# Performance work log

Measured on AMD Instinct MI355X. Metric: run time of the kernel, lower is better.

Reference implementation:

```python
import jax, jax.numpy as jnp
import numpy as np

B, C, W, H = 4, 256, 64, 64
CQ = C // 8


def setup_inputs() -> dict:
    key = jax.random.key(0)
    ks = jax.random.split(key, 8)
    s = 1.0 / np.sqrt(C)
    return {
        "x": jax.random.normal(ks[0], (B, C, W, H), dtype=jnp.float32),
        "Wq": jax.random.normal(ks[1], (CQ, C), dtype=jnp.float32) * s,
        "bq": jnp.zeros((CQ,), dtype=jnp.float32),
        "Wk": jax.random.normal(ks[2], (CQ, C), dtype=jnp.float32) * s,
        "bk": jnp.zeros((CQ,), dtype=jnp.float32),
        "Wv": jax.random.normal(ks[3], (C, C), dtype=jnp.float32) * s,
        "bv": jnp.zeros((C,), dtype=jnp.float32),
        "gamma": jnp.zeros((1,), dtype=jnp.float32),
    }


def reference(x, Wq, bq, Wk, bk, Wv, bv, gamma):
    b, c, w, h = x.shape
    n = w * h
    xf = x.reshape(b, c, n)  # [B, C, N] flattened spatial
    # 1x1 convs are channel-wise linear maps
    q = jnp.einsum("dc,bcn->bnd", Wq, xf) + bq  # [B, N, C//8]
    k = jnp.einsum("dc,bcn->bdn", Wk, xf) + bk[None, :, None]  # [B, C//8, N]
    v = jnp.einsum("dc,bcn->bdn", Wv, xf) + bv[None, :, None]  # [B, C, N]
    attn = jax.nn.softmax(jnp.einsum("bnd,bdm->bnm", q, k), axis=-1)  # [B, N, N]
    # out[b, c, n] = sum_m v[b, c, m] * attn[b, n, m]
    out = jnp.einsum("bdm,bnm->bdn", v, attn).reshape(b, c, w, h)
    return gamma[0] * out + x
```

## Files before the change

### kernel.cpp

```cpp
#include <hip/hip_runtime.h>
#include <hip/hip_bf16.h>

#define CC 256
#define NN 4096
#define CQ 32
#define LOG2E 1.4426950408889634f

using short8 = __attribute__((ext_vector_type(8))) short;
using f32x4  = __attribute__((ext_vector_type(4))) float;

static __device__ __forceinline__ short f2bf(float f) {
  __hip_bfloat16 h = __float2bfloat16(f);
  return *reinterpret_cast<short*>(&h);
}

__global__ __launch_bounds__(256) void prep_kernel(
    const float* __restrict__ Wq, const float* __restrict__ Wk,
    const float* __restrict__ Wv, __hip_bfloat16* __restrict__ Wf)
{
  int t = blockIdx.x*256 + threadIdx.x;
  int lane = t & 63, frag = t >> 6;
  int tile = frag >> 3, kc = frag & 7;
  int l15 = lane & 15, quad = lane >> 4;
  int R = tile*16 + l15;
  int k0 = kc*32 + quad*8;
  const float* src;
  if (R < 32)       src = Wq + (size_t)R*CC + k0;
  else if (R < 64)  src = Wk + (size_t)(R-32)*CC + k0;
  else              src = Wv + (size_t)(R-64)*CC + k0;
  float4 a = *(const float4*)(src);
  float4 c = *(const float4*)(src + 4);
  short8 o;
  o[0]=f2bf(a.x); o[1]=f2bf(a.y); o[2]=f2bf(a.z); o[3]=f2bf(a.w);
  o[4]=f2bf(c.x); o[5]=f2bf(c.y); o[6]=f2bf(c.z); o[7]=f2bf(c.w);
  *reinterpret_cast<short8*>(reinterpret_cast<short*>(Wf) + (size_t)t*8) = o;
}

__global__ __launch_bounds__(512, 2) void qkv_kernel(
    const float* __restrict__ x, const __hip_bfloat16* __restrict__ Wf,
    const float* __restrict__ bq, const float* __restrict__ bk,
    const float* __restrict__ bv,
    __hip_bfloat16* __restrict__ qb, __hip_bfloat16* __restrict__ kb,
    __hip_bfloat16* __restrict__ vb)
{
  const int b  = blockIdx.y;
  const int n0 = blockIdx.x * 64;
  const int tid = threadIdx.x;
  const int lane = tid & 63;
  const int w = __builtin_amdgcn_readfirstlane(tid >> 6);
  const int l15 = lane & 15, quad = lane >> 4;

  __shared__ __align__(16) short Xs[64][264];
  __shared__ __align__(16) short Vr[8][16][72];

  const int sn = tid & 63, cg8 = tid >> 6;
  const float* xcol = x + (size_t)b*CC*NN + n0 + sn;
#pragma unroll
  for (int it = 0; it < 4; it++) {
    int cbase = it*64 + cg8*8;
    float v[8];
#pragma unroll
    for (int j = 0; j < 8; j++) v[j] = xcol[(size_t)(cbase + j)*NN];
    short8 sv;
#pragma unroll
    for (int j = 0; j < 8; j++) sv[j] = f2bf(v[j]);
    *reinterpret_cast<short8*>(&Xs[sn][cbase]) = sv;
  }
  __syncthreads();

  const short* wfp = reinterpret_cast<const short*>(Wf);

#define QKV_TILE(T) { \
    const int t_ = (T); \
    short8 Af[8]; \
    _Pragma("unroll") \
    for (int kc = 0; kc < 8; kc++) \
      Af[kc] = *(const short8*)(wfp + ((size_t)(t_*8 + kc)*64 + lane)*8); \
    f32x4 ac0 = {0.f,0.f,0.f,0.f}, ac1 = {0.f,0.f,0.f,0.f}; \
    f32x4 ac2 = {0.f,0.f,0.f,0.f}, ac3 = {0.f,0.f,0.f,0.f}; \
    _Pragma("unroll") \
    for (int kc = 0; kc < 8; kc++) { \
      short8 B0 = *(const short8*)(&Xs[     l15][kc*32 + quad*8]); \
      short8 B1 = *(const short8*)(&Xs[16 + l15][kc*32 + quad*8]); \
      short8 B2 = *(const short8*)(&Xs[32 + l15][kc*32 + quad*8]); \
      short8 B3 = *(const short8*)(&Xs[48 + l15][kc*32 + quad*8]); \
      ac0 = __builtin_amdgcn_mfma_f32_16x16x32_bf16(Af[kc], B0, ac0, 0,0,0); \
      ac1 = __builtin_amdgcn_mfma_f32_16x16x32_bf16(Af[kc], B1, ac1, 0,0,0); \
      ac2 = __builtin_amdgcn_mfma_f32_16x16x32_bf16(Af[kc], B2, ac2, 0,0,0); \
      ac3 = __builtin_amdgcn_mfma_f32_16x16x32_bf16(Af[kc], B3, ac3, 0,0,0); \
    } \
    if (t_ < 2) { \
      int d0 = t_*16; \
      _Pragma("unroll") \
      for (int r = 0; r < 4; r++) { \
        int d = d0 + quad*4 + r; float bb = bq[d]; \
        qb[(size_t)b*NN*CQ + (size_t)(n0      + l15)*CQ + d] = __float2bfloat16(LOG2E*(ac0[r] + bb)); \
        qb[(size_t)b*NN*CQ + (size_t)(n0 + 16 + l15)*CQ + d] = __float2bfloat16(LOG2E*(ac1[r] + bb)); \
        qb[(size_t)b*NN*CQ + (size_t)(n0 + 32 + l15)*CQ + d] = __float2bfloat16(LOG2E*(ac2[r] + bb)); \
        qb[(size_t)b*NN*CQ + (size_t)(n0 + 48 + l15)*CQ + d] = __float2bfloat16(LOG2E*(ac3[r] + bb)); \
      } \
    } else if (t_ < 4) { \
      int d0 = (t_-2)*16; \
      _Pragma("unroll") \
      for (int r = 0; r < 4; r++) { \
        int d = d0 + quad*4 + r; float bb = bk[d]; \
        kb[(size_t)b*NN*CQ + (size_t)(n0      + l15)*CQ + d] = __float2bfloat16(ac0[r] + bb); \
        kb[(size_t)b*NN*CQ + (size_t)(n0 + 16 + l15)*CQ + d] = __float2bfloat16(ac1[r] + bb); \
        kb[(size_t)b*NN*CQ + (size_t)(n0 + 32 + l15)*CQ + d] = __float2bfloat16(ac2[r] + bb); \
        kb[(size_t)b*NN*CQ + (size_t)(n0 + 48 + l15)*CQ + d] = __float2bfloat16(ac3[r] + bb); \
      } \
    } else { \
      int rv0 = (t_-4)*16; \
      _Pragma("unroll") \
      for (int r = 0; r < 4; r++) { \
        float bb = bv[rv0 + quad*4 + r]; \
        Vr[w][quad*4 + r][     l15] = f2bf(ac0[r] + bb); \
        Vr[w][quad*4 + r][16 + l15] = f2bf(ac1[r] + bb); \
        Vr[w][quad*4 + r][32 + l15] = f2bf(ac2[r] + bb); \
        Vr[w][quad*4 + r][48 + l15] = f2bf(ac3[r] + bb); \
      } \
      int row = lane >> 2, cb = (lane & 3)*16; \
      short8 t0 = *(const short8*)(&Vr[w][row][cb]); \
      short8 t1 = *(const short8*)(&Vr[w][row][cb + 8]); \
      *(short8*)(vb + ((size_t)b*CC + rv0 + row)*NN + n0 + cb)     = t0; \
      *(short8*)(vb + ((size_t)b*CC + rv0 + row)*NN + n0 + cb + 8) = t1; \
    } }

  QKV_TILE(2*w);
  QKV_TILE(2*w + 1);
  if (w < 4) { QKV_TILE(16 + w); }
#undef QKV_TILE
}

__global__ __launch_bounds__(512, 2) void attn_kernel(
    const __hip_bfloat16* __restrict__ qb, const __hip_bfloat16* __restrict__ kb,
    const __hip_bfloat16* __restrict__ vb,
    const float* __restrict__ x, const float* __restrict__ gamma,
    float* __restrict__ out)
{
  const int Bk = blockIdx.x;
  const int b = (Bk & 7) >> 1;
  const int n0 = ((Bk >> 3)*2 + (Bk & 1)) * 64;
  const int tid = threadIdx.x;
  const int lane = tid & 63;
  const int w = __builtin_amdgcn_readfirstlane(tid >> 6);
  const int sg = w & 3;
  const int mh = w >> 2;
  const int l15 = lane & 15, quad = lane >> 4;

  __shared__ __align__(16) short Vs[256][72];
  __shared__ __align__(16) short Ps[64][72];
  __shared__ float Lbuf2[2][64];

  const short* qbase = (const short*)qb + (size_t)b*NN*CQ;
  const short* kbase = (const short*)kb + (size_t)b*NN*CQ;
  const short* vbase = (const short*)vb + (size_t)b*CC*NN;

  short8 aq = *(const short8*)(qbase + (size_t)(n0 + sg*16 + l15)*CQ + quad*8);

  const int vr = tid >> 1, sh = tid & 1;

  short8 vf0, vf1, vf2, vf3, kf0, kf1;
#pragma unroll
  for (int j = 0; j < 4; j++) {
    short8 t = *(const short8*)(vbase + (size_t)vr*NN + sh*32 + j*8);
    if (j == 0) vf0 = t; else if (j == 1) vf1 = t; else if (j == 2) vf2 = t; else vf3 = t;
  }
  kf0 = *(const short8*)(kbase + (size_t)(mh*32 +      l15)*CQ + quad*8);
  kf1 = *(const short8*)(kbase + (size_t)(mh*32 + 16 + l15)*CQ + quad*8);
  *(short8*)(&Vs[vr][sh*32 +  0]) = vf0;
  *(short8*)(&Vs[vr][sh*32 +  8]) = vf1;
  *(short8*)(&Vs[vr][sh*32 + 16]) = vf2;
  *(short8*)(&Vs[vr][sh*32 + 24]) = vf3;

  f32x4 acc[4][4];
#pragma unroll
  for (int cg = 0; cg < 4; cg++)
#pragma unroll
    for (int ng = 0; ng < 4; ng++) acc[cg][ng] = (f32x4){0.f,0.f,0.f,0.f};
  float lsum[4] = {0.f,0.f,0.f,0.f};

  __syncthreads();

  for (int T = 0; T < 64; T++) {
    short8 nv0, nv1, nv2, nv3, nk0, nk1;
    if (T < 63) {
      const short* vp = vbase + (size_t)vr*NN + (T+1)*64 + sh*32;
      nv0 = *(const short8*)(vp);
      nv1 = *(const short8*)(vp + 8);
      nv2 = *(const short8*)(vp + 16);
      nv3 = *(const short8*)(vp + 24);
      nk0 = *(const short8*)(kbase + (size_t)((T+1)*64 + mh*32 +      l15)*CQ + quad*8);
      nk1 = *(const short8*)(kbase + (size_t)((T+1)*64 + mh*32 + 16 + l15)*CQ + quad*8);
    }

    f32x4 z = {0.f,0.f,0.f,0.f};
    f32x4 S0 = __builtin_amdgcn_mfma_f32_16x16x32_bf16(aq, kf0, z, 0,0,0);
    f32x4 S1 = __builtin_amdgcn_mfma_f32_16x16x32_bf16(aq, kf1, z, 0,0,0);
#pragma unroll
    for (int r = 0; r < 4; r++) {
      float e0 = __builtin_amdgcn_exp2f(S0[r]);
      float e1 = __builtin_amdgcn_exp2f(S1[r]);
      lsum[r] += e0 + e1;
      Ps[sg*16 + quad*4 + r][mh*32 +      l15] = f2bf(e0);
      Ps[sg*16 + quad*4 + r][mh*32 + 16 + l15] = f2bf(e1);
    }
    __syncthreads();

    short8 ap0 = *(const short8*)(&Ps[     l15][mh*32 + quad*8]);
    short8 ap1 = *(const short8*)(&Ps[16 + l15][mh*32 + quad*8]);
    short8 ap2 = *(const short8*)(&Ps[32 + l15][mh*32 + quad*8]);
    short8 ap3 = *(const short8*)(&Ps[48 + l15][mh*32 + quad*8]);
#pragma unroll
    for (int cg = 0; cg < 4; cg++) {
      short8 av = *(const short8*)(&Vs[sg*64 + cg*16 + l15][mh*32 + quad*8]);
      acc[cg][0] = __builtin_amdgcn_mfma_f32_16x16x32_bf16(av, ap0, acc[cg][0], 0,0,0);
      acc[cg][1] = __builtin_amdgcn_mfma_f32_16x16x32_bf16(av, ap1, acc[cg][1], 0,0,0);
      acc[cg][2] = __builtin_amdgcn_mfma_f32_16x16x32_bf16(av, ap2, acc[cg][2], 0,0,0);
      acc[cg][3] = __builtin_amdgcn_mfma_f32_16x16x32_bf16(av, ap3, acc[cg][3], 0,0,0);
    }
    __syncthreads();

    if (T < 63) {
      *(short8*)(&Vs[vr][sh*32 +  0]) = nv0;
      *(short8*)(&Vs[vr][sh*32 +  8]) = nv1;
      *(short8*)(&Vs[vr][sh*32 + 16]) = nv2;
      *(short8*)(&Vs[vr][sh*32 + 24]) = nv3;
      kf0 = nk0; kf1 = nk1;
    }
  }

#pragma unroll
  for (int r = 0; r < 4; r++) {
    float s = lsum[r];
    s += __shfl_xor(s, 1); s += __shfl_xor(s, 2);
    s += __shfl_xor(s, 4); s += __shfl_xor(s, 8);
    if (l15 == 0) Lbuf2[mh][sg*16 + quad*4 + r] = s;
  }

  float* poolf = reinterpret_cast<float*>(&Vs[0][0]);
  __syncthreads();
#pragma unroll
  for (int g = 0; g < 2; g++) {
    if (mh == 1 && (sg >> 1) == g) {
#pragma unroll
      for (int cg = 0; cg < 4; cg++)
#pragma unroll
        for (int ng = 0; ng < 4; ng++)
#pragma unroll
          for (int r = 0; r < 4; r++)
            poolf[(sg & 1)*4096 + (cg*16 + quad*4 + r)*64 + ng*16 + l15] = acc[cg][ng][r];
    }
    __syncthreads();
    if (mh == 0 && (sg >> 1) == g) {
#pragma unroll
      for (int cg = 0; cg < 4; cg++)
#pragma unroll
        for (int ng = 0; ng < 4; ng++)
#pragma unroll
          for (int r = 0; r < 4; r++)
            acc[cg][ng][r] += poolf[(sg & 1)*4096 + (cg*16 + quad*4 + r)*64 + ng*16 + l15];
    }
    __syncthreads();
  }

  if (mh == 0) {
    const float gm = gamma[0];
    float Lv[4];
#pragma unroll
    for (int ng = 0; ng < 4; ng++)
      Lv[ng] = 1.0f / (Lbuf2[0][ng*16 + l15] + Lbuf2[1][ng*16 + l15]);
#pragma unroll
    for (int cg = 0; cg < 4; cg++) {
#pragma unroll
      for (int ng = 0; ng < 4; ng++) {
#pragma unroll
        for (int r = 0; r < 4; r++) {
          size_t idx = ((size_t)b*CC + sg*64 + cg*16 + quad*4 + r)*NN + n0 + ng*16 + l15;
          out[idx] = gm * acc[cg][ng][r] * Lv[ng] + x[idx];
        }
      }
    }
  }
}

extern "C" void kernel_launch(void* const* d_in, const int* in_sizes, int n_in,
                              void* d_out, int out_size, void* d_ws, size_t ws_size,
                              hipStream_t stream) {
  const float* x     = (const float*)d_in[0];
  const float* Wq    = (const float*)d_in[1];
  const float* bq    = (const float*)d_in[2];
  const float* Wk    = (const float*)d_in[3];
  const float* bk    = (const float*)d_in[4];
  const float* Wv    = (const float*)d_in[5];
  const float* bv    = (const float*)d_in[6];
  const float* gamma = (const float*)d_in[7];
  float* out = (float*)d_out;

  char* ws = (char*)d_ws;
  if (ws_size < (11u << 20)) return;
  __hip_bfloat16* qb = (__hip_bfloat16*)(ws);
  __hip_bfloat16* kb = (__hip_bfloat16*)(ws + (1u << 20));
  __hip_bfloat16* vb = (__hip_bfloat16*)(ws + (2u << 20));
  __hip_bfloat16* Wf = (__hip_bfloat16*)(ws + (10u << 20));

  prep_kernel<<<dim3(40), 256, 0, stream>>>(Wq, Wk, Wv, Wf);
  qkv_kernel<<<dim3(64, 4), 512, 0, stream>>>(x, Wf, bq, bk, bv, qb, kb, vb);
  attn_kernel<<<dim3(256), 512, 0, stream>>>(qb, kb, vb, x, gamma, out);
}
```

Measured before the change: 155.1 us.

## Restructure QKV projection into smaller blocks with fragment-ordered LDS and vector stores

The QKV projection kernel now processes 32 spatial positions per 256-thread block instead of 64 per 512 threads, doubling the grid to 512 blocks. x is staged into LDS directly in MFMA fragment order so each B operand is one contiguous 16-byte read, and q/k outputs are packed into 4-element bf16 vector stores instead of scalar stores. The intent is more blocks for occupancy and cheaper LDS and global writes. In exchange, each block reloads the full weight fragments for half as much work, and V stores become narrower 16-byte rows.

Result: faster. 151.6 us (-2.2%).

```diff
diff --git a/kernel.cpp b/kernel.cpp
--- a/kernel.cpp
+++ b/kernel.cpp
@@ -6,6 +6,7 @@
 #define CQ 32
 #define LOG2E 1.4426950408889634f
 
+using short4v = __attribute__((ext_vector_type(4))) short;
 using short8 = __attribute__((ext_vector_type(8))) short;
 using f32x4  = __attribute__((ext_vector_type(4))) float;
 
@@ -36,7 +37,7 @@
   *reinterpret_cast<short8*>(reinterpret_cast<short*>(Wf) + (size_t)t*8) = o;
 }
 
-__global__ __launch_bounds__(512, 2) void qkv_kernel(
+__global__ __launch_bounds__(256) void qkv_kernel(
     const float* __restrict__ x, const __hip_bfloat16* __restrict__ Wf,
     const float* __restrict__ bq, const float* __restrict__ bk,
     const float* __restrict__ bv,
@@ -44,31 +45,38 @@
     __hip_bfloat16* __restrict__ vb)
 {
   const int b  = blockIdx.y;
-  const int n0 = blockIdx.x * 64;
+  const int n0 = blockIdx.x * 32;
   const int tid = threadIdx.x;
   const int lane = tid & 63;
   const int w = __builtin_amdgcn_readfirstlane(tid >> 6);
   const int l15 = lane & 15, quad = lane >> 4;
 
-  __shared__ __align__(16) short Xs[64][264];
-  __shared__ __align__(16) short Vr[8][16][72];
-
-  const int sn = tid & 63, cg8 = tid >> 6;
-  const float* xcol = x + (size_t)b*CC*NN + n0 + sn;
-#pragma unroll
-  for (int it = 0; it < 4; it++) {
-    int cbase = it*64 + cg8*8;
+  __shared__ __align__(16) short Xl[16*64*8];
+  __shared__ __align__(16) short Vr[4][16][32];
+
+  const float* xb = x + (size_t)b*CC*NN;
+#pragma unroll
+  for (int i = 0; i < 4; i++) {
+    int s = tid + 256*i;
+    int g = s >> 6, ln = s & 63;
+    int nr = g >> 3, kc = g & 7;
+    int l15s = ln & 15, quads = ln >> 4;
+    int n = n0 + nr*16 + l15s;
+    int c0 = kc*32 + quads*8;
     float v[8];
 #pragma unroll
-    for (int j = 0; j < 8; j++) v[j] = xcol[(size_t)(cbase + j)*NN];
+    for (int j = 0; j < 8; j++) v[j] = xb[(size_t)(c0 + j)*NN + n];
     short8 sv;
 #pragma unroll
     for (int j = 0; j < 8; j++) sv[j] = f2bf(v[j]);
-    *reinterpret_cast<short8*>(&Xs[sn][cbase]) = sv;
+    *reinterpret_cast<short8*>(&Xl[(size_t)s*8]) = sv;
   }
   __syncthreads();
 
   const short* wfp = reinterpret_cast<const short*>(Wf);
+  short* qb_s = reinterpret_cast<short*>(qb) + (size_t)b*NN*CQ;
+  short* kb_s = reinterpret_cast<short*>(kb) + (size_t)b*NN*CQ;
+  short* vb_s = reinterpret_cast<short*>(vb) + (size_t)b*CC*NN;
 
 #define QKV_TILE(T) { \
     const int t_ = (T); \
@@ -77,38 +85,35 @@
     for (int kc = 0; kc < 8; kc++) \
       Af[kc] = *(const short8*)(wfp + ((size_t)(t_*8 + kc)*64 + lane)*8); \
     f32x4 ac0 = {0.f,0.f,0.f,0.f}, ac1 = {0.f,0.f,0.f,0.f}; \
-    f32x4 ac2 = {0.f,0.f,0.f,0.f}, ac3 = {0.f,0.f,0.f,0.f}; \
     _Pragma("unroll") \
     for (int kc = 0; kc < 8; kc++) { \
-      short8 B0 = *(const short8*)(&Xs[     l15][kc*32 + quad*8]); \
-      short8 B1 = *(const short8*)(&Xs[16 + l15][kc*32 + quad*8]); \
-      short8 B2 = *(const short8*)(&Xs[32 + l15][kc*32 + quad*8]); \
-      short8 B3 = *(const short8*)(&Xs[48 + l15][kc*32 + quad*8]); \
+      short8 B0 = *(const short8*)(&Xl[((     kc)*64 + lane)*8]); \
+      short8 B1 = *(const short8*)(&Xl[((8 +  kc)*64 + lane)*8]); \
       ac0 = __builtin_amdgcn_mfma_f32_16x16x32_bf16(Af[kc], B0, ac0, 0,0,0); \
       ac1 = __builtin_amdgcn_mfma_f32_16x16x32_bf16(Af[kc], B1, ac1, 0,0,0); \
-      ac2 = __builtin_amdgcn_mfma_f32_16x16x32_bf16(Af[kc], B2, ac2, 0,0,0); \
-      ac3 = __builtin_amdgcn_mfma_f32_16x16x32_bf16(Af[kc], B3, ac3, 0,0,0); \
     } \
     if (t_ < 2) { \
-      int d0 = t_*16; \
+      int d0 = t_*16 + quad*4; \
+      short4v p0, p1; \
       _Pragma("unroll") \
       for (int r = 0; r < 4; r++) { \
-        int d = d0 + quad*4 + r; float bb = bq[d]; \
-        qb[(size_t)b*NN*CQ + (size_t)(n0      + l15)*CQ + d] = __float2bfloat16(LOG2E*(ac0[r] + bb)); \
-        qb[(size_t)b*NN*CQ + (size_t)(n0 + 16 + l15)*CQ + d] = __float2bfloat16(LOG2E*(ac1[r] + bb)); \
-        qb[(size_t)b*NN*CQ + (size_t)(n0 + 32 + l15)*CQ + d] = __float2bfloat16(LOG2E*(ac2[r] + bb)); \
-        qb[(size_t)b*NN*CQ + (size_t)(n0 + 48 + l15)*CQ + d] = __float2bfloat16(LOG2E*(ac3[r] + bb)); \
+        float bb = bq[d0 + r]; \
+        p0[r] = f2bf(LOG2E*(ac0[r] + bb)); \
+        p1[r] = f2bf(LOG2E*(ac1[r] + bb)); \
       } \
+      *(short4v*)(qb_s + (size_t)(n0      + l15)*CQ + d0) = p0; \
+      *(short4v*)(qb_s + (size_t)(n0 + 16 + l15)*CQ + d0) = p1; \
     } else if (t_ < 4) { \
-      int d0 = (t_-2)*16; \
+      int d0 = (t_-2)*16 + quad*4; \
+      short4v p0, p1; \
       _Pragma("unroll") \
       for (int r = 0; r < 4; r++) { \
-        int d = d0 + quad*4 + r; float bb = bk[d]; \
-        kb[(size_t)b*NN*CQ + (size_t)(n0      + l15)*CQ + d] = __float2bfloat16(ac0[r] + bb); \
-        kb[(size_t)b*NN*CQ + (size_t)(n0 + 16 + l15)*CQ + d] = __float2bfloat16(ac1[r] + bb); \
-        kb[(size_t)b*NN*CQ + (size_t)(n0 + 32 + l15)*CQ + d] = __float2bfloat16(ac2[r] + bb); \
-        kb[(size_t)b*NN*CQ + (size_t)(n0 + 48 + l15)*CQ + d] = __float2bfloat16(ac3[r] + bb); \
+        float bb = bk[d0 + r]; \
+        p0[r] = f2bf(ac0[r] + bb); \
+        p1[r] = f2bf(ac1[r] + bb); \
       } \
+      *(short4v*)(kb_s + (size_t)(n0      + l15)*CQ + d0) = p0; \
+      *(short4v*)(kb_s + (size_t)(n0 + 16 + l15)*CQ + d0) = p1; \
     } else { \
       int rv0 = (t_-4)*16; \
       _Pragma("unroll") \
@@ -116,19 +121,17 @@
         float bb = bv[rv0 + quad*4 + r]; \
         Vr[w][quad*4 + r][     l15] = f2bf(ac0[r] + bb); \
         Vr[w][quad*4 + r][16 + l15] = f2bf(ac1[r] + bb); \
-        Vr[w][quad*4 + r][32 + l15] = f2bf(ac2[r] + bb); \
-        Vr[w][quad*4 + r][48 + l15] = f2bf(ac3[r] + bb); \
       } \
-      int row = lane >> 2, cb = (lane & 3)*16; \
-      short8 t0 = *(const short8*)(&Vr[w][row][cb]); \
-      short8 t1 = *(const short8*)(&Vr[w][row][cb + 8]); \
-      *(short8*)(vb + ((size_t)b*CC + rv0 + row)*NN + n0 + cb)     = t0; \
-      *(short8*)(vb + ((size_t)b*CC + rv0 + row)*NN + n0 + cb + 8) = t1; \
+      int row = lane >> 2, cb = (lane & 3)*8; \
+      short8 tv = *(const short8*)(&Vr[w][row][cb]); \
+      *(short8*)(vb_s + (size_t)(rv0 + row)*NN + n0 + cb) = tv; \
     } }
 
-  QKV_TILE(2*w);
-  QKV_TILE(2*w + 1);
-  if (w < 4) { QKV_TILE(16 + w); }
+  QKV_TILE(w);
+  QKV_TILE(4 + w);
+  QKV_TILE(8 + w);
+  QKV_TILE(12 + w);
+  QKV_TILE(16 + w);
 #undef QKV_TILE
 }
 
@@ -305,6 +308,6 @@
   __hip_bfloat16* Wf = (__hip_bfloat16*)(ws + (10u << 20));
 
   prep_kernel<<<dim3(40), 256, 0, stream>>>(Wq, Wk, Wv, Wf);
-  qkv_kernel<<<dim3(64, 4), 512, 0, stream>>>(x, Wf, bq, bk, bv, qb, kb, vb);
+  qkv_kernel<<<dim3(128, 4), 256, 0, stream>>>(x, Wf, bq, bk, bv, qb, kb, vb);
   attn_kernel<<<dim3(256), 512, 0, stream>>>(qb, kb, vb, x, gamma, out);
 }
```
